# Optimization experiments

Measured on AMD Instinct MI355X. Metric: run time of the kernel, lower is better.

The kernel has to match this reference:

```python
import jax, jax.numpy as jnp
import numpy as np

B, T, D, H, P = 2, 2048, 1024, 16, 64  # batch, seq, d_model, heads, head_dim


def setup_inputs() -> dict:
    key = jax.random.key(0)
    ks = jax.random.split(key, 8)
    s = 0.02
    return {
        "Q": jax.random.normal(ks[0], (B, T, D), jnp.float32),
        "K": jax.random.normal(ks[1], (B, T, D), jnp.float32),
        "V": jax.random.normal(ks[2], (B, T, D), jnp.float32),
        "mask": jnp.ones((B, 1, 1, T), jnp.float32),
        "WQ": jax.random.normal(ks[3], (H, D, P), jnp.float32) * s,
        "WK": jax.random.normal(ks[4], (H, D, P), jnp.float32) * s,
        "WV": jax.random.normal(ks[5], (H, D, P), jnp.float32) * s,
        "rel_emb": jax.random.normal(ks[6], (2 * T - 1, P), jnp.float32) * s,
        "dense_W": jax.random.normal(ks[7], (H * P, D), jnp.float32) * s,
        "dense_b": jnp.zeros((D,), jnp.float32),
    }


def reference(Q, K, V, mask, WQ, WK, WV, rel_emb, dense_W, dense_b):
    # multi-head projections: (B,T,D) x (H,D,P) -> (B,H,T,P)
    q = jnp.einsum("btd,hdp->bhtp", Q, WQ)
    k = jnp.einsum("btd,hdp->bhtp", K, WK)
    v = jnp.einsum("btd,hdp->bhtp", V, WV)

    Tq = q.shape[2]
    # Shaw-style additive relative positional encoding from Q:
    # bias[b,h,i,j] = q[b,h,i] . rel_emb[j - i + T - 1]
    a = jnp.einsum("bhtp,rp->bhtr", q, rel_emb)          # (B,H,T,2T-1)
    rel_idx = jnp.arange(Tq)[None, :] - jnp.arange(Tq)[:, None] + (Tq - 1)  # (T,T)
    rpe = jnp.take_along_axis(a, rel_idx[None, None], axis=-1)              # (B,H,T,T)

    scale = 1.0 / jnp.sqrt(jnp.asarray(P, q.dtype))
    energies = (jnp.einsum("bhtp,bhsp->bhts", q, k) + rpe) * scale
    energies = energies + (1.0 - mask) * -1e9
    alphas = jax.nn.softmax(energies, axis=-1)
    ctx = jnp.einsum("bhts,bhsp->bhtp", alphas, v)        # (B,H,T,P)

    ctx = jnp.transpose(ctx, (0, 2, 1, 3)).reshape(ctx.shape[0], Tq, H * P)
    return ctx @ dense_W + dense_b
```

## Files before the change

kernel.cpp:

```cpp
#include <hip/hip_runtime.h>
#include <hip/hip_bf16.h>

typedef __bf16 bf16_t;
typedef __bf16 bf16x2 __attribute__((ext_vector_type(2)));
typedef __bf16 bf16x8 __attribute__((ext_vector_type(8)));
typedef float f32x4 __attribute__((ext_vector_type(4)));

#define QSCALE 0.1803368801111396f
#define MLOG2E 1.4426950408889634f
#define MCONST 12.0f

__device__ __forceinline__ f32x4 mfma16(bf16x8 a, bf16x8 b, f32x4 c) {
  return __builtin_amdgcn_mfma_f32_16x16x32_bf16(a, b, c, 0, 0, 0);
}

#define GLDS16(gsrc, ldst)                                                     \
  __builtin_amdgcn_global_load_lds(                                            \
      (const __attribute__((address_space(1))) void*)(gsrc),                   \
      (__attribute__((address_space(3))) void*)(ldst), 16, 0, 0)

__device__ __forceinline__ unsigned pack2(float a, float b) {
  bf16x2 t = {(bf16_t)a, (bf16_t)b};
  return __builtin_bit_cast(unsigned, t);
}

__global__ void prep_kernel(const float* __restrict__ rel,
                            const float* __restrict__ mask,
                            bf16_t* __restrict__ relb,
                            float* __restrict__ mbias) {
  int idx = blockIdx.x * 256 + threadIdx.x;
  if (idx < 4096 * 64) {
    int row = idx >> 6;
    int col = idx & 63;
    int sr = row > 4094 ? 4094 : row;
    relb[idx] = (bf16_t)rel[sr * 64 + col];
  } else {
    int j = idx - 4096 * 64;
    if (j < 4096) mbias[j] = (1.0f - mask[j]) * -1e9f * MLOG2E;
  }
}

__global__ __launch_bounds__(256) void proj_gemm_kernel(
    const float* __restrict__ Q, const float* __restrict__ K,
    const float* __restrict__ V, const float* __restrict__ WQ,
    const float* __restrict__ WK, const float* __restrict__ WV,
    bf16_t* __restrict__ qb, bf16_t* __restrict__ kb,
    bf16_t* __restrict__ vb) {
  const int z = blockIdx.z;
  const float* A = z == 0 ? Q : (z == 1 ? K : V);
  const float* W = z == 0 ? WQ : (z == 1 ? WK : WV);
  bf16_t* out = z == 0 ? qb : (z == 1 ? kb : vb);
  const float scale = z == 0 ? QSCALE : 1.0f;

  __shared__ bf16_t As[128][72];
  __shared__ bf16_t Bs[128][72];
  const int tid = threadIdx.x;
  const int lane = tid & 63;
  const int wid = tid >> 6;
  const int wm = wid >> 1, wn = wid & 1;
  const int row0 = blockIdx.x * 128;
  const int col0 = blockIdx.y * 128;
  const int lr = lane & 15;
  const int lk = (lane >> 4) * 8;

  f32x4 acc[4][4];
#pragma unroll
  for (int m = 0; m < 4; m++)
#pragma unroll
    for (int n = 0; n < 4; n++) acc[m][n] = {0.f, 0.f, 0.f, 0.f};

  for (int kt = 0; kt < 1024; kt += 64) {
#pragma unroll
    for (int i = 0; i < 4; i++) {
      int c = tid + i * 256;
      int row = c >> 3;
      int k8 = (c & 7) * 8;
      const float* src = A + (size_t)(row0 + row) * 1024 + kt + k8;
      float4 v0 = *(const float4*)(src);
      float4 v1 = *(const float4*)(src + 4);
      uint4 u = {pack2(v0.x, v0.y), pack2(v0.z, v0.w), pack2(v1.x, v1.y),
                 pack2(v1.z, v1.w)};
      *(uint4*)&As[row][k8] = u;
    }
#pragma unroll
    for (int i = 0; i < 4; i++) {
      int c = tid + i * 256;
      int col = c & 127;
      int k8 = (c >> 7) * 8;
      int gcol = col0 + col;
      int h = gcol >> 6, p = gcol & 63;
      const float* src = W + (size_t)h * 65536 + (size_t)(kt + k8) * 64 + p;
      float w0 = src[0], w1 = src[64], w2 = src[128], w3 = src[192];
      float w4 = src[256], w5 = src[320], w6 = src[384], w7 = src[448];
      uint4 u = {pack2(w0, w1), pack2(w2, w3), pack2(w4, w5), pack2(w6, w7)};
      *(uint4*)&Bs[col][k8] = u;
    }
    __syncthreads();
#pragma unroll
    for (int kk = 0; kk < 2; kk++) {
      bf16x8 af[4], bfr[4];
#pragma unroll
      for (int m = 0; m < 4; m++)
        af[m] = *(const bf16x8*)&As[wm * 64 + m * 16 + lr][kk * 32 + lk];
#pragma unroll
      for (int n = 0; n < 4; n++)
        bfr[n] = *(const bf16x8*)&Bs[wn * 64 + n * 16 + lr][kk * 32 + lk];
#pragma unroll
      for (int m = 0; m < 4; m++)
#pragma unroll
        for (int n = 0; n < 4; n++)
          acc[m][n] = mfma16(af[m], bfr[n], acc[m][n]);
    }
    __syncthreads();
  }
  const int rb = (lane >> 4) * 4;
#pragma unroll
  for (int m = 0; m < 4; m++) {
#pragma unroll
    for (int n = 0; n < 4; n++) {
      int col = col0 + wn * 64 + n * 16 + lr;
      int h = col >> 6, p = col & 63;
      int row_base = row0 + wm * 64 + m * 16 + rb;
      int b = row_base >> 11, t0 = row_base & 2047;
      if (z == 2) {
        uint2 u = {pack2(acc[m][n][0], acc[m][n][1]),
                   pack2(acc[m][n][2], acc[m][n][3])};
        *(uint2*)&out[(((size_t)(b * 16 + h) * 64 + p) * 2048) + t0] = u;
      } else {
#pragma unroll
        for (int r = 0; r < 4; r++) {
          out[(((size_t)(b * 16 + h) * 2048 + t0 + r) * 64) + p] =
              (bf16_t)(acc[m][n][r] * scale);
        }
      }
    }
  }
}

__global__ __launch_bounds__(256) void dense_gemm_kernel(
    const bf16_t* __restrict__ A, const float* __restrict__ W,
    const float* __restrict__ bias, float* __restrict__ out) {
  __shared__ bf16_t As[128][72];
  __shared__ bf16_t Bs[128][72];
  const int tid = threadIdx.x;
  const int lane = tid & 63;
  const int wid = tid >> 6;
  const int wm = wid >> 1, wn = wid & 1;
  const int row0 = blockIdx.x * 128;
  const int col0 = blockIdx.y * 128;
  const int lr = lane & 15;
  const int lk = (lane >> 4) * 8;

  f32x4 acc[4][4];
#pragma unroll
  for (int m = 0; m < 4; m++)
#pragma unroll
    for (int n = 0; n < 4; n++) acc[m][n] = {0.f, 0.f, 0.f, 0.f};

  for (int kt = 0; kt < 1024; kt += 64) {
#pragma unroll
    for (int i = 0; i < 4; i++) {
      int c = tid + i * 256;
      int row = c >> 3;
      int k8 = (c & 7) * 8;
      *(uint4*)&As[row][k8] =
          *(const uint4*)(A + (size_t)(row0 + row) * 1024 + kt + k8);
    }
#pragma unroll
    for (int i = 0; i < 4; i++) {
      int c = tid + i * 256;
      int col = c & 127;
      int k8 = (c >> 7) * 8;
      const float* src = W + (size_t)(kt + k8) * 1024 + col0 + col;
      float w0 = src[0], w1 = src[1024], w2 = src[2048], w3 = src[3072];
      float w4 = src[4096], w5 = src[5120], w6 = src[6144], w7 = src[7168];
      uint4 u = {pack2(w0, w1), pack2(w2, w3), pack2(w4, w5), pack2(w6, w7)};
      *(uint4*)&Bs[col][k8] = u;
    }
    __syncthreads();
#pragma unroll
    for (int kk = 0; kk < 2; kk++) {
      bf16x8 af[4], bfr[4];
#pragma unroll
      for (int m = 0; m < 4; m++)
        af[m] = *(const bf16x8*)&As[wm * 64 + m * 16 + lr][kk * 32 + lk];
#pragma unroll
      for (int n = 0; n < 4; n++)
        bfr[n] = *(const bf16x8*)&Bs[wn * 64 + n * 16 + lr][kk * 32 + lk];
#pragma unroll
      for (int m = 0; m < 4; m++)
#pragma unroll
        for (int n = 0; n < 4; n++)
          acc[m][n] = mfma16(af[m], bfr[n], acc[m][n]);
    }
    __syncthreads();
  }
  const int rb = (lane >> 4) * 4;
#pragma unroll
  for (int m = 0; m < 4; m++) {
#pragma unroll
    for (int n = 0; n < 4; n++) {
      int col = col0 + wn * 64 + n * 16 + lr;
      float bv = bias[col];
#pragma unroll
      for (int r = 0; r < 4; r++) {
        int row = row0 + wm * 64 + m * 16 + rb + r;
        out[(size_t)row * 1024 + col] = acc[m][n][r] + bv;
      }
    }
  }
}

__global__ __launch_bounds__(256, 2) void attn_kernel(
    const bf16_t* __restrict__ qg, const bf16_t* __restrict__ kg,
    const bf16_t* __restrict__ vt, const bf16_t* __restrict__ relb,
    const float* __restrict__ mbias, bf16_t* __restrict__ ctx) {
  __shared__ bf16_t Kb[2][64 * 64];
  __shared__ bf16_t Vb[2][64 * 64];
  __shared__ bf16_t Rr[4][64 * 64];
  __shared__ unsigned SC[4][688];

  const int tid = threadIdx.x;
  const int lane = tid & 63;
  const int w = tid >> 6;

  const int id = blockIdx.x;
  const int id2 = (id & 7) * 64 + (id >> 3);
  const int it = id2 & 15;
  const int bh = id2 >> 4;
  const int h = bh & 15;
  const int b = bh >> 4;
  const int i0 = it * 128;

  const size_t base = ((size_t)bh) * 2048 * 64;
  const int lr = lane & 15;
  const int g = lane >> 4;
  const int lk = g * 8;
  const int srow = lane >> 3;
  const int t16 = lane & 7;
  const int swz = (lr & 7) << 3;

  const bf16_t* kgb = kg + base;
  const bf16_t* vgb = vt + base;
  const bf16_t* rgb = relb + (size_t)(1920 - i0) * 64;

  bf16x8 aq[2][2];
#pragma unroll
  for (int gq = 0; gq < 2; gq++) {
    const bf16_t* src =
        qg + base + (size_t)(i0 + w * 32 + gq * 16 + lr) * 64 + lk;
    aq[gq][0] = *(const bf16x8*)(src);
    aq[gq][1] = *(const bf16x8*)(src + 32);
  }

  float l0 = 0.f, l1 = 0.f;
  f32x4 o0[4], o1[4];
#pragma unroll
  for (int n = 0; n < 4; n++) {
    o0[n] = {0.f, 0.f, 0.f, 0.f};
    o1[n] = {0.f, 0.f, 0.f, 0.f};
  }

  const float* mb_base = mbias + (size_t)b * 2048;
  unsigned* scw = SC[w];
  int sh[4];
#pragma unroll
  for (int r = 0; r < 4; r++) sh[r] = ((r + lr + 1) & 1) << 4;

#pragma unroll
  for (int i = 0; i < 2; i++) {
    int chunk = i * 4 + w;
    int row = chunk * 8 + srow;
    GLDS16(kgb + row * 64 + ((t16 ^ (row & 7)) * 8),
           Kb[0] + chunk * 512 + lane * 8);
  }
#pragma unroll
  for (int i = 0; i < 2; i++) {
    int chunk = i * 4 + w;
    int p = chunk * 8 + srow;
    GLDS16(vgb + (size_t)p * 2048 + ((t16 ^ (p & 7)) * 8),
           Vb[0] + chunk * 512 + lane * 8);
  }
#pragma unroll
  for (int c = 0; c < 3; c++) {
#pragma unroll
    for (int i = 0; i < 2; i++) {
      int chunk = i * 4 + w;
      int row = chunk * 8 + srow;
      GLDS16(rgb + (size_t)(c * 64 + row) * 64 + ((t16 ^ (row & 7)) * 8),
             Rr[c] + chunk * 512 + lane * 8);
    }
  }
  __syncthreads();

  for (int jt = 0; jt < 32; jt++) {
    const int j0 = jt * 64;

    f32x4 mbv[4];
#pragma unroll
    for (int n = 0; n < 4; n++)
      mbv[n] = *(const f32x4*)&mb_base[j0 + n * 16 + g * 4];

    if (jt < 31) {
#pragma unroll
      for (int i = 0; i < 2; i++) {
        int chunk = i * 4 + w;
        int p = chunk * 8 + srow;
        GLDS16(vgb + (j0 + 64) + (size_t)p * 2048 + ((t16 ^ (p & 7)) * 8),
               Vb[(jt + 1) & 1] + chunk * 512 + lane * 8);
      }
      const bf16_t* kn = kgb + (size_t)(j0 + 64) * 64;
      bf16_t* kd = Kb[(jt + 1) & 1];
#pragma unroll
      for (int i = 0; i < 2; i++) {
        int chunk = i * 4 + w;
        int row = chunk * 8 + srow;
        GLDS16(kn + row * 64 + ((t16 ^ (row & 7)) * 8),
               kd + chunk * 512 + lane * 8);
      }
      const bf16_t* rs = rgb + (size_t)(jt + 3) * 64 * 64;
      bf16_t* rd = Rr[(jt + 3) & 3];
#pragma unroll
      for (int i = 0; i < 2; i++) {
        int chunk = i * 4 + w;
        int row = chunk * 8 + srow;
        GLDS16(rs + row * 64 + ((t16 ^ (row & 7)) * 8),
               rd + chunk * 512 + lane * 8);
      }
    }

    f32x4 sacc0[4], sacc1[4], er0[5], er1[5];
#pragma unroll
    for (int n = 0; n < 4; n++) {
      sacc0[n] = {0.f, 0.f, 0.f, 0.f};
      sacc1[n] = {0.f, 0.f, 0.f, 0.f};
    }
#pragma unroll
    for (int n = 0; n < 5; n++) {
      er0[n] = {0.f, 0.f, 0.f, 0.f};
      er1[n] = {0.f, 0.f, 0.f, 0.f};
    }
    const bf16_t* kcur = Kb[jt & 1];
    __builtin_amdgcn_s_setprio(1);
#pragma unroll
    for (int kk = 0; kk < 2; kk++) {
      int cbs = (kk * 32 + lk) ^ swz;
#pragma unroll
      for (int n = 0; n < 4; n++) {
        bf16x8 ak = *(const bf16x8*)&kcur[(n * 16 + lr) * 64 + cbs];
        sacc0[n] = mfma16(ak, aq[0][kk], sacc0[n]);
        sacc1[n] = mfma16(ak, aq[1][kk], sacc1[n]);
      }
#pragma unroll
      for (int fi = 0; fi < 6; fi++) {
        int f = 6 - 2 * w + fi;
        const bf16_t* rc = Rr[(jt + (f >> 2)) & 3];
        bf16x8 ar = *(const bf16x8*)&rc[((f & 3) * 16 + lr) * 64 + cbs];
        if (fi >= 1) er0[fi - 1] = mfma16(ar, aq[0][kk], er0[fi - 1]);
        if (fi <= 4) er1[fi] = mfma16(ar, aq[1][kk], er1[fi]);
      }
    }
    __builtin_amdgcn_s_setprio(0);

    bf16x8 bp0[2], bp1[2];
#pragma unroll
    for (int gq = 0; gq < 2; gq++) {
      f32x4* sacc = gq ? sacc1 : sacc0;
      f32x4* er = gq ? er1 : er0;
#pragma unroll
      for (int n2 = 0; n2 < 5; n2++) {
        uint2 u = {pack2(er[n2][0], er[n2][1]), pack2(er[n2][2], er[n2][3])};
        *(uint2*)&scw[lr * 42 + n2 * 8 + g * 2] = u;
      }
      float ps = 0.f;
      float e[4][4];
#pragma unroll
      for (int n = 0; n < 4; n++) {
#pragma unroll
        for (int r = 0; r < 4; r++) {
          int key = n * 16 + g * 4 + r;
          int idx = key - lr + 15;
          unsigned d = scw[lr * 42 + (idx >> 1)];
          float bias = __builtin_bit_cast(float, (d >> sh[r]) << 16);
          float s = sacc[n][r] + bias + mbv[n][r];
          e[n][r] = exp2f(s - MCONST);
          ps += e[n][r];
        }
      }
      if (gq) l1 += ps; else l0 += ps;
#pragma unroll
      for (int n = 0; n < 4; n++) {
        uint2 u = {pack2(e[n][0], e[n][1]), pack2(e[n][2], e[n][3])};
        *(uint2*)&scw[lr * 36 + n * 8 + g * 2] = u;
      }
      uint4 t0 = *(const uint4*)&scw[lr * 36 + g * 4];
      uint4 t1 = *(const uint4*)&scw[lr * 36 + 16 + g * 4];
      if (gq) {
        bp1[0] = __builtin_bit_cast(bf16x8, t0);
        bp1[1] = __builtin_bit_cast(bf16x8, t1);
      } else {
        bp0[0] = __builtin_bit_cast(bf16x8, t0);
        bp0[1] = __builtin_bit_cast(bf16x8, t1);
      }
    }

    const bf16_t* vcur = Vb[jt & 1];
    __builtin_amdgcn_s_setprio(1);
#pragma unroll
    for (int kk = 0; kk < 2; kk++) {
      int cbs = (kk * 32 + lk) ^ swz;
#pragma unroll
      for (int n = 0; n < 4; n++) {
        bf16x8 av = *(const bf16x8*)&vcur[(n * 16 + lr) * 64 + cbs];
        o0[n] = mfma16(av, bp0[kk], o0[n]);
        o1[n] = mfma16(av, bp1[kk], o1[n]);
      }
    }
    __builtin_amdgcn_s_setprio(0);

    __syncthreads();
  }

  l0 += __shfl_xor(l0, 16, 64);
  l0 += __shfl_xor(l0, 32, 64);
  l1 += __shfl_xor(l1, 16, 64);
  l1 += __shfl_xor(l1, 32, 64);

#pragma unroll
  for (int gq = 0; gq < 2; gq++) {
    f32x4* o = gq ? o1 : o0;
    float inv = 1.0f / (gq ? l1 : l0);
    size_t bt = (size_t)b * 2048 + i0 + w * 32 + gq * 16 + lr;
#pragma unroll
    for (int n = 0; n < 4; n++) {
      uint2 u = {pack2(o[n][0] * inv, o[n][1] * inv),
                 pack2(o[n][2] * inv, o[n][3] * inv)};
      *(uint2*)&ctx[bt * 1024 + h * 64 + n * 16 + g * 4] = u;
    }
  }
}

extern "C" void kernel_launch(void* const* d_in, const int* in_sizes, int n_in,
                              void* d_out, int out_size, void* d_ws,
                              size_t ws_size, hipStream_t stream) {
  (void)in_sizes; (void)n_in; (void)out_size; (void)ws_size;
  const float* Q    = (const float*)d_in[0];
  const float* K    = (const float*)d_in[1];
  const float* V    = (const float*)d_in[2];
  const float* mask = (const float*)d_in[3];
  const float* WQ   = (const float*)d_in[4];
  const float* WK   = (const float*)d_in[5];
  const float* WV   = (const float*)d_in[6];
  const float* rel  = (const float*)d_in[7];
  const float* dW   = (const float*)d_in[8];
  const float* db   = (const float*)d_in[9];
  float* out = (float*)d_out;

  const size_t NQKV = (size_t)2 * 16 * 2048 * 64;
  bf16_t* qb   = (bf16_t*)d_ws;
  bf16_t* kb   = qb + NQKV;
  bf16_t* vb   = kb + NQKV;
  bf16_t* ctxb = vb + NQKV;
  bf16_t* relb = ctxb + NQKV;
  float*  mbias = (float*)(relb + 4096 * 64);

  dim3 blk(256);
  prep_kernel<<<dim3((4096 * 64 + 4096) / 256), blk, 0, stream>>>(rel, mask,
                                                                  relb, mbias);
  proj_gemm_kernel<<<dim3(32, 8, 3), blk, 0, stream>>>(Q, K, V, WQ, WK, WV, qb,
                                                       kb, vb);
  attn_kernel<<<dim3(512), blk, 0, stream>>>(qb, kb, vb, relb, mbias, ctxb);
  dense_gemm_kernel<<<dim3(32, 8), blk, 0, stream>>>(ctxb, dW, db, out);
}
```

Baseline: 193.0 us.

## Split attention over key tiles with atomic accumulation and deferred normalisation

The attention grid triples from 512 to 1536 blocks, and each block handles roughly a third of the key tiles. Partial unnormalised outputs and row sums are accumulated into fp32 buffers with atomicAdd, after a memset. The dense GEMM now reads the fp32 context, divides by the accumulated sum and converts to bf16 while loading. The relative-embedding tile is read straight from global into registers instead of staged in LDS, which frees shared memory for 3 blocks per CU. The softmax uses a fixed max constant rather than a running max, so summing partials across splits stays correct. The cost is heavy float atomic traffic (64 atomics per row per block), a larger fp32 intermediate and an extra memset.

```diff
diff --git a/kernel.cpp b/kernel.cpp
--- a/kernel.cpp
+++ b/kernel.cpp
@@ -138,8 +138,9 @@
 }
 
 __global__ __launch_bounds__(256) void dense_gemm_kernel(
-    const bf16_t* __restrict__ A, const float* __restrict__ W,
-    const float* __restrict__ bias, float* __restrict__ out) {
+    const float* __restrict__ octx, const float* __restrict__ lbuf,
+    const float* __restrict__ W, const float* __restrict__ bias,
+    float* __restrict__ out) {
   __shared__ bf16_t As[128][72];
   __shared__ bf16_t Bs[128][72];
   const int tid = threadIdx.x;
@@ -161,10 +162,18 @@
 #pragma unroll
     for (int i = 0; i < 4; i++) {
       int c = tid + i * 256;
-      int row = c >> 3;
+      int row = row0 + (c >> 3);
       int k8 = (c & 7) * 8;
-      *(uint4*)&As[row][k8] =
-          *(const uint4*)(A + (size_t)(row0 + row) * 1024 + kt + k8);
+      int gk = kt + k8;
+      const float* src = octx + (size_t)row * 1024 + gk;
+      float invl =
+          1.0f / lbuf[(size_t)(((row >> 11) << 4) + (gk >> 6)) * 2048 +
+                      (row & 2047)];
+      float4 v0 = *(const float4*)(src);
+      float4 v1 = *(const float4*)(src + 4);
+      uint4 u = {pack2(v0.x * invl, v0.y * invl), pack2(v0.z * invl, v0.w * invl),
+                 pack2(v1.x * invl, v1.y * invl), pack2(v1.z * invl, v1.w * invl)};
+      *(uint4*)&As[c >> 3][k8] = u;
     }
 #pragma unroll
     for (int i = 0; i < 4; i++) {
@@ -211,13 +220,13 @@
   }
 }
 
-__global__ __launch_bounds__(256, 2) void attn_kernel(
+__global__ __launch_bounds__(256, 3) void attn_kernel(
     const bf16_t* __restrict__ qg, const bf16_t* __restrict__ kg,
     const bf16_t* __restrict__ vt, const bf16_t* __restrict__ relb,
-    const float* __restrict__ mbias, bf16_t* __restrict__ ctx) {
+    const float* __restrict__ mbias, float* __restrict__ octx,
+    float* __restrict__ lbuf) {
   __shared__ bf16_t Kb[2][64 * 64];
   __shared__ bf16_t Vb[2][64 * 64];
-  __shared__ bf16_t Rr[4][64 * 64];
   __shared__ unsigned SC[4][688];
 
   const int tid = threadIdx.x;
@@ -225,12 +234,16 @@
   const int w = tid >> 6;
 
   const int id = blockIdx.x;
-  const int id2 = (id & 7) * 64 + (id >> 3);
+  const int sidx = id >> 9;
+  const int rid = id & 511;
+  const int id2 = (rid & 7) * 64 + (rid >> 3);
   const int it = id2 & 15;
   const int bh = id2 >> 4;
   const int h = bh & 15;
   const int b = bh >> 4;
   const int i0 = it * 128;
+  const int jt0 = sidx * 11;
+  const int jt1 = sidx == 2 ? 32 : jt0 + 11;
 
   const size_t base = ((size_t)bh) * 2048 * 64;
   const int lr = lane & 15;
@@ -242,7 +255,7 @@
 
   const bf16_t* kgb = kg + base;
   const bf16_t* vgb = vt + base;
-  const bf16_t* rgb = relb + (size_t)(1920 - i0) * 64;
+  const bf16_t* rgb = relb + (size_t)(1920 - i0) * 64 + lk;
 
   bf16x8 aq[2][2];
 #pragma unroll
@@ -271,61 +284,51 @@
   for (int i = 0; i < 2; i++) {
     int chunk = i * 4 + w;
     int row = chunk * 8 + srow;
-    GLDS16(kgb + row * 64 + ((t16 ^ (row & 7)) * 8),
+    GLDS16(kgb + (size_t)(jt0 * 64 + row) * 64 + ((t16 ^ (row & 7)) * 8),
            Kb[0] + chunk * 512 + lane * 8);
   }
 #pragma unroll
   for (int i = 0; i < 2; i++) {
     int chunk = i * 4 + w;
     int p = chunk * 8 + srow;
-    GLDS16(vgb + (size_t)p * 2048 + ((t16 ^ (p & 7)) * 8),
+    GLDS16(vgb + jt0 * 64 + (size_t)p * 2048 + ((t16 ^ (p & 7)) * 8),
            Vb[0] + chunk * 512 + lane * 8);
   }
-#pragma unroll
-  for (int c = 0; c < 3; c++) {
-#pragma unroll
-    for (int i = 0; i < 2; i++) {
-      int chunk = i * 4 + w;
-      int row = chunk * 8 + srow;
-      GLDS16(rgb + (size_t)(c * 64 + row) * 64 + ((t16 ^ (row & 7)) * 8),
-             Rr[c] + chunk * 512 + lane * 8);
-    }
-  }
   __syncthreads();
 
-  for (int jt = 0; jt < 32; jt++) {
+  int lt = 0;
+  for (int jt = jt0; jt < jt1; ++jt, ++lt) {
     const int j0 = jt * 64;
+    const int cur = lt & 1;
 
     f32x4 mbv[4];
 #pragma unroll
     for (int n = 0; n < 4; n++)
       mbv[n] = *(const f32x4*)&mb_base[j0 + n * 16 + g * 4];
 
-    if (jt < 31) {
+    const bf16_t* rb0 = rgb + (size_t)j0 * 64;
+    bf16x8 ar0[6];
+#pragma unroll
+    for (int fi = 0; fi < 6; fi++) {
+      int f = 6 - 2 * w + fi;
+      ar0[fi] = *(const bf16x8*)(rb0 + (size_t)(f * 16 + lr) * 64);
+    }
+
+    if (jt + 1 < jt1) {
 #pragma unroll
       for (int i = 0; i < 2; i++) {
         int chunk = i * 4 + w;
         int p = chunk * 8 + srow;
         GLDS16(vgb + (j0 + 64) + (size_t)p * 2048 + ((t16 ^ (p & 7)) * 8),
-               Vb[(jt + 1) & 1] + chunk * 512 + lane * 8);
+               Vb[cur ^ 1] + chunk * 512 + lane * 8);
       }
       const bf16_t* kn = kgb + (size_t)(j0 + 64) * 64;
-      bf16_t* kd = Kb[(jt + 1) & 1];
 #pragma unroll
       for (int i = 0; i < 2; i++) {
         int chunk = i * 4 + w;
         int row = chunk * 8 + srow;
         GLDS16(kn + row * 64 + ((t16 ^ (row & 7)) * 8),
-               kd + chunk * 512 + lane * 8);
-      }
-      const bf16_t* rs = rgb + (size_t)(jt + 3) * 64 * 64;
-      bf16_t* rd = Rr[(jt + 3) & 3];
-#pragma unroll
-      for (int i = 0; i < 2; i++) {
-        int chunk = i * 4 + w;
-        int row = chunk * 8 + srow;
-        GLDS16(rs + row * 64 + ((t16 ^ (row & 7)) * 8),
-               rd + chunk * 512 + lane * 8);
+               Kb[cur ^ 1] + chunk * 512 + lane * 8);
       }
     }
 
@@ -340,25 +343,41 @@
       er0[n] = {0.f, 0.f, 0.f, 0.f};
       er1[n] = {0.f, 0.f, 0.f, 0.f};
     }
-    const bf16_t* kcur = Kb[jt & 1];
+    const bf16_t* kcur = Kb[cur];
     __builtin_amdgcn_s_setprio(1);
-#pragma unroll
-    for (int kk = 0; kk < 2; kk++) {
-      int cbs = (kk * 32 + lk) ^ swz;
+    {
+      int cbs = lk ^ swz;
 #pragma unroll
       for (int n = 0; n < 4; n++) {
         bf16x8 ak = *(const bf16x8*)&kcur[(n * 16 + lr) * 64 + cbs];
-        sacc0[n] = mfma16(ak, aq[0][kk], sacc0[n]);
-        sacc1[n] = mfma16(ak, aq[1][kk], sacc1[n]);
-      }
-#pragma unroll
-      for (int fi = 0; fi < 6; fi++) {
-        int f = 6 - 2 * w + fi;
-        const bf16_t* rc = Rr[(jt + (f >> 2)) & 3];
-        bf16x8 ar = *(const bf16x8*)&rc[((f & 3) * 16 + lr) * 64 + cbs];
-        if (fi >= 1) er0[fi - 1] = mfma16(ar, aq[0][kk], er0[fi - 1]);
-        if (fi <= 4) er1[fi] = mfma16(ar, aq[1][kk], er1[fi]);
-      }
+        sacc0[n] = mfma16(ak, aq[0][0], sacc0[n]);
+        sacc1[n] = mfma16(ak, aq[1][0], sacc1[n]);
+      }
+    }
+    bf16x8 ar1[6];
+#pragma unroll
+    for (int fi = 0; fi < 6; fi++) {
+      int f = 6 - 2 * w + fi;
+      ar1[fi] = *(const bf16x8*)(rb0 + 32 + (size_t)(f * 16 + lr) * 64);
+    }
+#pragma unroll
+    for (int fi = 0; fi < 6; fi++) {
+      if (fi >= 1) er0[fi - 1] = mfma16(ar0[fi], aq[0][0], er0[fi - 1]);
+      if (fi <= 4) er1[fi] = mfma16(ar0[fi], aq[1][0], er1[fi]);
+    }
+    {
+      int cbs = (32 + lk) ^ swz;
+#pragma unroll
+      for (int n = 0; n < 4; n++) {
+        bf16x8 ak = *(const bf16x8*)&kcur[(n * 16 + lr) * 64 + cbs];
+        sacc0[n] = mfma16(ak, aq[0][1], sacc0[n]);
+        sacc1[n] = mfma16(ak, aq[1][1], sacc1[n]);
+      }
+    }
+#pragma unroll
+    for (int fi = 0; fi < 6; fi++) {
+      if (fi >= 1) er0[fi - 1] = mfma16(ar1[fi], aq[0][1], er0[fi - 1]);
+      if (fi <= 4) er1[fi] = mfma16(ar1[fi], aq[1][1], er1[fi]);
     }
     __builtin_amdgcn_s_setprio(0);
 
@@ -404,7 +423,7 @@
       }
     }
 
-    const bf16_t* vcur = Vb[jt & 1];
+    const bf16_t* vcur = Vb[cur];
     __builtin_amdgcn_s_setprio(1);
 #pragma unroll
     for (int kk = 0; kk < 2; kk++) {
@@ -429,13 +448,14 @@
 #pragma unroll
   for (int gq = 0; gq < 2; gq++) {
     f32x4* o = gq ? o1 : o0;
-    float inv = 1.0f / (gq ? l1 : l0);
-    size_t bt = (size_t)b * 2048 + i0 + w * 32 + gq * 16 + lr;
+    int q = i0 + w * 32 + gq * 16 + lr;
+    if (g == 0) atomicAdd(&lbuf[(size_t)bh * 2048 + q], gq ? l1 : l0);
+    size_t bt = (size_t)b * 2048 + q;
+    float* dst = octx + bt * 1024 + h * 64 + g * 4;
 #pragma unroll
     for (int n = 0; n < 4; n++) {
-      uint2 u = {pack2(o[n][0] * inv, o[n][1] * inv),
-                 pack2(o[n][2] * inv, o[n][3] * inv)};
-      *(uint2*)&ctx[bt * 1024 + h * 64 + n * 16 + g * 4] = u;
+#pragma unroll
+      for (int r = 0; r < 4; r++) atomicAdd(dst + n * 16 + r, o[n][r]);
     }
   }
 }
@@ -460,15 +480,19 @@
   bf16_t* qb   = (bf16_t*)d_ws;
   bf16_t* kb   = qb + NQKV;
   bf16_t* vb   = kb + NQKV;
-  bf16_t* ctxb = vb + NQKV;
-  bf16_t* relb = ctxb + NQKV;
+  bf16_t* relb = vb + NQKV;
   float*  mbias = (float*)(relb + 4096 * 64);
+  float*  octx = mbias + 4096;
+  float*  lbuf = octx + (size_t)4096 * 1024;
 
   dim3 blk(256);
   prep_kernel<<<dim3((4096 * 64 + 4096) / 256), blk, 0, stream>>>(rel, mask,
                                                                   relb, mbias);
   proj_gemm_kernel<<<dim3(32, 8, 3), blk, 0, stream>>>(Q, K, V, WQ, WK, WV, qb,
                                                        kb, vb);
-  attn_kernel<<<dim3(512), blk, 0, stream>>>(qb, kb, vb, relb, mbias, ctxb);
-  dense_gemm_kernel<<<dim3(32, 8), blk, 0, stream>>>(ctxb, dW, db, out);
-}
+  hipMemsetAsync(octx, 0, ((size_t)4096 * 1024 + 2 * 16 * 2048) * sizeof(float),
+                 stream);
+  attn_kernel<<<dim3(1536), blk, 0, stream>>>(qb, kb, vb, relb, mbias, octx,
+                                              lbuf);
+  dense_gemm_kernel<<<dim3(32, 8), blk, 0, stream>>>(octx, lbuf, dW, db, out);
+}
```

Result: slower. 571.6 us (+196.2%).

## Pre-convert fp32 inputs and weights to bf16, interleave softmax with PV MFMAs

Applied to the files above, without the earlier changes.

Adds a separate conversion kernel that casts Q, K, V and all weight matrices to bf16 in workspace, so the projection and dense GEMMs read half-width data instead of converting fp32 inside their tile loads. The attention loop is also restructured so the softmax of the second query group is computed after the first group's PV MFMAs, with V fragments loaded once and reused. The extra pass adds a full read of fp32 inputs plus a bf16 write and re-read. Weight loads in the GEMMs remain strided scalar loads, now of 2-byte elements.

```diff
diff --git a/kernel.cpp b/kernel.cpp
--- a/kernel.cpp
+++ b/kernel.cpp
@@ -22,6 +22,42 @@
 __device__ __forceinline__ unsigned pack2(float a, float b) {
   bf16x2 t = {(bf16_t)a, (bf16_t)b};
   return __builtin_bit_cast(unsigned, t);
+}
+__device__ __forceinline__ unsigned short bbits(bf16_t v) {
+  return __builtin_bit_cast(unsigned short, v);
+}
+
+__global__ void conv_kernel(const float* __restrict__ Q,
+                            const float* __restrict__ K,
+                            const float* __restrict__ V,
+                            const float* __restrict__ WQ,
+                            const float* __restrict__ WK,
+                            const float* __restrict__ WV,
+                            const float* __restrict__ dW,
+                            bf16_t* __restrict__ qf, bf16_t* __restrict__ kf,
+                            bf16_t* __restrict__ vf, bf16_t* __restrict__ wqf,
+                            bf16_t* __restrict__ wkf, bf16_t* __restrict__ wvf,
+                            bf16_t* __restrict__ dwf) {
+  const int y = blockIdx.y;
+  const float* s;
+  bf16_t* d;
+  size_t n;
+  switch (y) {
+    case 0: s = Q;  d = qf;  n = 4194304; break;
+    case 1: s = K;  d = kf;  n = 4194304; break;
+    case 2: s = V;  d = vf;  n = 4194304; break;
+    case 3: s = WQ; d = wqf; n = 1048576; break;
+    case 4: s = WK; d = wkf; n = 1048576; break;
+    case 5: s = WV; d = wvf; n = 1048576; break;
+    default: s = dW; d = dwf; n = 1048576; break;
+  }
+  size_t i = ((size_t)blockIdx.x * 256 + threadIdx.x) * 8;
+  if (i >= n) return;
+  float4 a = *(const float4*)(s + i);
+  float4 b = *(const float4*)(s + i + 4);
+  uint4 u = {pack2(a.x, a.y), pack2(a.z, a.w), pack2(b.x, b.y),
+             pack2(b.z, b.w)};
+  *(uint4*)(d + i) = u;
 }
 
 __global__ void prep_kernel(const float* __restrict__ rel,
@@ -41,14 +77,14 @@
 }
 
 __global__ __launch_bounds__(256) void proj_gemm_kernel(
-    const float* __restrict__ Q, const float* __restrict__ K,
-    const float* __restrict__ V, const float* __restrict__ WQ,
-    const float* __restrict__ WK, const float* __restrict__ WV,
+    const bf16_t* __restrict__ Qf, const bf16_t* __restrict__ Kf,
+    const bf16_t* __restrict__ Vf, const bf16_t* __restrict__ WQf,
+    const bf16_t* __restrict__ WKf, const bf16_t* __restrict__ WVf,
     bf16_t* __restrict__ qb, bf16_t* __restrict__ kb,
     bf16_t* __restrict__ vb) {
   const int z = blockIdx.z;
-  const float* A = z == 0 ? Q : (z == 1 ? K : V);
-  const float* W = z == 0 ? WQ : (z == 1 ? WK : WV);
+  const bf16_t* A = z == 0 ? Qf : (z == 1 ? Kf : Vf);
+  const bf16_t* W = z == 0 ? WQf : (z == 1 ? WKf : WVf);
   bf16_t* out = z == 0 ? qb : (z == 1 ? kb : vb);
   const float scale = z == 0 ? QSCALE : 1.0f;
 
@@ -75,12 +111,8 @@
       int c = tid + i * 256;
       int row = c >> 3;
       int k8 = (c & 7) * 8;
-      const float* src = A + (size_t)(row0 + row) * 1024 + kt + k8;
-      float4 v0 = *(const float4*)(src);
-      float4 v1 = *(const float4*)(src + 4);
-      uint4 u = {pack2(v0.x, v0.y), pack2(v0.z, v0.w), pack2(v1.x, v1.y),
-                 pack2(v1.z, v1.w)};
-      *(uint4*)&As[row][k8] = u;
+      *(uint4*)&As[row][k8] =
+          *(const uint4*)(A + (size_t)(row0 + row) * 1024 + kt + k8);
     }
 #pragma unroll
     for (int i = 0; i < 4; i++) {
@@ -89,10 +121,15 @@
       int k8 = (c >> 7) * 8;
       int gcol = col0 + col;
       int h = gcol >> 6, p = gcol & 63;
-      const float* src = W + (size_t)h * 65536 + (size_t)(kt + k8) * 64 + p;
-      float w0 = src[0], w1 = src[64], w2 = src[128], w3 = src[192];
-      float w4 = src[256], w5 = src[320], w6 = src[384], w7 = src[448];
-      uint4 u = {pack2(w0, w1), pack2(w2, w3), pack2(w4, w5), pack2(w6, w7)};
+      const bf16_t* src = W + (size_t)h * 65536 + (size_t)(kt + k8) * 64 + p;
+      unsigned short b0 = bbits(src[0]), b1 = bbits(src[64]);
+      unsigned short b2 = bbits(src[128]), b3 = bbits(src[192]);
+      unsigned short b4 = bbits(src[256]), b5 = bbits(src[320]);
+      unsigned short b6 = bbits(src[384]), b7 = bbits(src[448]);
+      uint4 u = {(unsigned)b0 | ((unsigned)b1 << 16),
+                 (unsigned)b2 | ((unsigned)b3 << 16),
+                 (unsigned)b4 | ((unsigned)b5 << 16),
+                 (unsigned)b6 | ((unsigned)b7 << 16)};
       *(uint4*)&Bs[col][k8] = u;
     }
     __syncthreads();
@@ -138,7 +175,7 @@
 }
 
 __global__ __launch_bounds__(256) void dense_gemm_kernel(
-    const bf16_t* __restrict__ A, const float* __restrict__ W,
+    const bf16_t* __restrict__ A, const bf16_t* __restrict__ W,
     const float* __restrict__ bias, float* __restrict__ out) {
   __shared__ bf16_t As[128][72];
   __shared__ bf16_t Bs[128][72];
@@ -171,10 +208,15 @@
       int c = tid + i * 256;
       int col = c & 127;
       int k8 = (c >> 7) * 8;
-      const float* src = W + (size_t)(kt + k8) * 1024 + col0 + col;
-      float w0 = src[0], w1 = src[1024], w2 = src[2048], w3 = src[3072];
-      float w4 = src[4096], w5 = src[5120], w6 = src[6144], w7 = src[7168];
-      uint4 u = {pack2(w0, w1), pack2(w2, w3), pack2(w4, w5), pack2(w6, w7)};
+      const bf16_t* src = W + (size_t)(kt + k8) * 1024 + col0 + col;
+      unsigned short b0 = bbits(src[0]), b1 = bbits(src[1024]);
+      unsigned short b2 = bbits(src[2048]), b3 = bbits(src[3072]);
+      unsigned short b4 = bbits(src[4096]), b5 = bbits(src[5120]);
+      unsigned short b6 = bbits(src[6144]), b7 = bbits(src[7168]);
+      uint4 u = {(unsigned)b0 | ((unsigned)b1 << 16),
+                 (unsigned)b2 | ((unsigned)b3 << 16),
+                 (unsigned)b4 | ((unsigned)b5 << 16),
+                 (unsigned)b6 | ((unsigned)b7 << 16)};
       *(uint4*)&Bs[col][k8] = u;
     }
     __syncthreads();
@@ -362,14 +404,13 @@
     }
     __builtin_amdgcn_s_setprio(0);
 
-    bf16x8 bp0[2], bp1[2];
-#pragma unroll
-    for (int gq = 0; gq < 2; gq++) {
-      f32x4* sacc = gq ? sacc1 : sacc0;
-      f32x4* er = gq ? er1 : er0;
+    const bf16_t* vcur = Vb[jt & 1];
+    bf16x8 av[2][4];
+
+    {
 #pragma unroll
       for (int n2 = 0; n2 < 5; n2++) {
-        uint2 u = {pack2(er[n2][0], er[n2][1]), pack2(er[n2][2], er[n2][3])};
+        uint2 u = {pack2(er0[n2][0], er0[n2][1]), pack2(er0[n2][2], er0[n2][3])};
         *(uint2*)&scw[lr * 42 + n2 * 8 + g * 2] = u;
       }
       float ps = 0.f;
@@ -382,41 +423,74 @@
           int idx = key - lr + 15;
           unsigned d = scw[lr * 42 + (idx >> 1)];
           float bias = __builtin_bit_cast(float, (d >> sh[r]) << 16);
-          float s = sacc[n][r] + bias + mbv[n][r];
+          float s = sacc0[n][r] + bias + mbv[n][r];
           e[n][r] = exp2f(s - MCONST);
           ps += e[n][r];
         }
       }
-      if (gq) l1 += ps; else l0 += ps;
+      l0 += ps;
 #pragma unroll
       for (int n = 0; n < 4; n++) {
         uint2 u = {pack2(e[n][0], e[n][1]), pack2(e[n][2], e[n][3])};
         *(uint2*)&scw[lr * 36 + n * 8 + g * 2] = u;
       }
-      uint4 t0 = *(const uint4*)&scw[lr * 36 + g * 4];
-      uint4 t1 = *(const uint4*)&scw[lr * 36 + 16 + g * 4];
-      if (gq) {
-        bp1[0] = __builtin_bit_cast(bf16x8, t0);
-        bp1[1] = __builtin_bit_cast(bf16x8, t1);
-      } else {
-        bp0[0] = __builtin_bit_cast(bf16x8, t0);
-        bp0[1] = __builtin_bit_cast(bf16x8, t1);
-      }
-    }
-
-    const bf16_t* vcur = Vb[jt & 1];
-    __builtin_amdgcn_s_setprio(1);
-#pragma unroll
-    for (int kk = 0; kk < 2; kk++) {
-      int cbs = (kk * 32 + lk) ^ swz;
+      bf16x8 bp0[2];
+      bp0[0] = __builtin_bit_cast(bf16x8, *(const uint4*)&scw[lr * 36 + g * 4]);
+      bp0[1] =
+          __builtin_bit_cast(bf16x8, *(const uint4*)&scw[lr * 36 + 16 + g * 4]);
+#pragma unroll
+      for (int kk = 0; kk < 2; kk++) {
+        int cbs = (kk * 32 + lk) ^ swz;
+#pragma unroll
+        for (int n = 0; n < 4; n++)
+          av[kk][n] = *(const bf16x8*)&vcur[(n * 16 + lr) * 64 + cbs];
+      }
+      __builtin_amdgcn_s_setprio(1);
+#pragma unroll
+      for (int kk = 0; kk < 2; kk++)
+#pragma unroll
+        for (int n = 0; n < 4; n++) o0[n] = mfma16(av[kk][n], bp0[kk], o0[n]);
+      __builtin_amdgcn_s_setprio(0);
+    }
+
+    {
+#pragma unroll
+      for (int n2 = 0; n2 < 5; n2++) {
+        uint2 u = {pack2(er1[n2][0], er1[n2][1]), pack2(er1[n2][2], er1[n2][3])};
+        *(uint2*)&scw[lr * 42 + n2 * 8 + g * 2] = u;
+      }
+      float ps = 0.f;
+      float e[4][4];
 #pragma unroll
       for (int n = 0; n < 4; n++) {
-        bf16x8 av = *(const bf16x8*)&vcur[(n * 16 + lr) * 64 + cbs];
-        o0[n] = mfma16(av, bp0[kk], o0[n]);
-        o1[n] = mfma16(av, bp1[kk], o1[n]);
-      }
-    }
-    __builtin_amdgcn_s_setprio(0);
+#pragma unroll
+        for (int r = 0; r < 4; r++) {
+          int key = n * 16 + g * 4 + r;
+          int idx = key - lr + 15;
+          unsigned d = scw[lr * 42 + (idx >> 1)];
+          float bias = __builtin_bit_cast(float, (d >> sh[r]) << 16);
+          float s = sacc1[n][r] + bias + mbv[n][r];
+          e[n][r] = exp2f(s - MCONST);
+          ps += e[n][r];
+        }
+      }
+      l1 += ps;
+#pragma unroll
+      for (int n = 0; n < 4; n++) {
+        uint2 u = {pack2(e[n][0], e[n][1]), pack2(e[n][2], e[n][3])};
+        *(uint2*)&scw[lr * 36 + n * 8 + g * 2] = u;
+      }
+      bf16x8 bp1[2];
+      bp1[0] = __builtin_bit_cast(bf16x8, *(const uint4*)&scw[lr * 36 + g * 4]);
+      bp1[1] =
+          __builtin_bit_cast(bf16x8, *(const uint4*)&scw[lr * 36 + 16 + g * 4]);
+      __builtin_amdgcn_s_setprio(1);
+#pragma unroll
+      for (int kk = 0; kk < 2; kk++)
+#pragma unroll
+        for (int n = 0; n < 4; n++) o1[n] = mfma16(av[kk][n], bp1[kk], o1[n]);
+      __builtin_amdgcn_s_setprio(0);
+    }
 
     __syncthreads();
   }
@@ -456,19 +530,29 @@
   const float* db   = (const float*)d_in[9];
   float* out = (float*)d_out;
 
-  const size_t NQKV = (size_t)2 * 16 * 2048 * 64;
-  bf16_t* qb   = (bf16_t*)d_ws;
-  bf16_t* kb   = qb + NQKV;
-  bf16_t* vb   = kb + NQKV;
-  bf16_t* ctxb = vb + NQKV;
-  bf16_t* relb = ctxb + NQKV;
+  const size_t N4M = (size_t)4096 * 1024;
+  const size_t N1M = (size_t)1024 * 1024;
+  bf16_t* qf   = (bf16_t*)d_ws;
+  bf16_t* kf   = qf + N4M;
+  bf16_t* vf   = kf + N4M;
+  bf16_t* wqf  = vf + N4M;
+  bf16_t* wkf  = wqf + N1M;
+  bf16_t* wvf  = wkf + N1M;
+  bf16_t* dwf  = wvf + N1M;
+  bf16_t* qb   = dwf + N1M;
+  bf16_t* kb   = qb + N4M;
+  bf16_t* vb   = kb + N4M;
+  bf16_t* ctxb = vb + N4M;
+  bf16_t* relb = ctxb + N4M;
   float*  mbias = (float*)(relb + 4096 * 64);
 
   dim3 blk(256);
+  conv_kernel<<<dim3(2048, 7), blk, 0, stream>>>(Q, K, V, WQ, WK, WV, dW, qf,
+                                                 kf, vf, wqf, wkf, wvf, dwf);
   prep_kernel<<<dim3((4096 * 64 + 4096) / 256), blk, 0, stream>>>(rel, mask,
                                                                   relb, mbias);
-  proj_gemm_kernel<<<dim3(32, 8, 3), blk, 0, stream>>>(Q, K, V, WQ, WK, WV, qb,
-                                                       kb, vb);
+  proj_gemm_kernel<<<dim3(32, 8, 3), blk, 0, stream>>>(qf, kf, vf, wqf, wkf,
+                                                       wvf, qb, kb, vb);
   attn_kernel<<<dim3(512), blk, 0, stream>>>(qb, kb, vb, relb, mbias, ctxb);
-  dense_gemm_kernel<<<dim3(32, 8), blk, 0, stream>>>(ctxb, dW, db, out);
-}
+  dense_gemm_kernel<<<dim3(32, 8), blk, 0, stream>>>(ctxb, dwf, db, out);
+}
```

Result: no change. 194.2 us (+0.6%).
